# Optimization experiments

Measured on AMD Instinct MI355X. Metric: run time of the kernel, lower is better.

The kernel has to match this reference:

```python
import jax, jax.numpy as jnp
import numpy as np


def _mlp(x, ws, bs):
    # Linear->ReLU between layers, final Linear has no activation
    for i, (w, b) in enumerate(zip(ws, bs)):
        x = x @ w + b
        if i < len(ws) - 1:
            x = jax.nn.relu(x)
    return x


def setup_inputs() -> dict:
    key = jax.random.key(0)
    ks = jax.random.split(key, 24)
    n, q, H, W, dim = 2, 131072, 64, 2048, 64
    num = 4
    depth = jax.random.normal(ks[0], (n, 3, H, W), dtype=jnp.float32)
    feat = jax.random.normal(ks[1], (n, dim, H, W), dtype=jnp.float32)
    coord = jax.random.uniform(ks[2], (n, q, 2), dtype=jnp.float32, minval=-1.0, maxval=1.0)

    def lin(k, din, dout):
        kw, kb = jax.random.split(k)
        s = 1.0 / np.sqrt(din)
        w = jax.random.uniform(kw, (din, dout), minval=-s, maxval=s, dtype=jnp.float32)
        b = jax.random.uniform(kb, (dout,), minval=-s, maxval=s, dtype=jnp.float32)
        return w, b

    # pos_embedd: 2*num=8 -> [dim, num//2*dim] = [64,128] -> num*dim=256
    pe_dims = [2 * num, dim, (num // 2) * dim, num * dim]
    # encoder_xy: num*dim=256 -> [num*dim, num//2*dim, dim] = [256,128,64] -> num=4
    enc_dims = [num * dim, num * dim, (num // 2) * dim, dim, num]
    inp = {"depth": depth, "feat": feat, "coord": coord}
    for i in range(3):
        w, b = lin(ks[3 + i], pe_dims[i], pe_dims[i + 1])
        inp[f"pe_w{i}"] = w
        inp[f"pe_b{i}"] = b
    for i in range(4):
        w, b = lin(ks[8 + i], enc_dims[i], enc_dims[i + 1])
        inp[f"enc_w{i}"] = w
        inp[f"enc_b{i}"] = b
    return inp


def reference(depth, feat, coord,
              pe_w0, pe_b0, pe_w1, pe_b1, pe_w2, pe_b2,
              enc_w0, enc_b0, enc_w1, enc_b1, enc_w2, enc_b2, enc_w3, enc_b3):
    n, C, H, W = feat.shape
    q = coord.shape[1]
    eps = 1e-6
    # xy range-view magnitude map [n, H, W]
    xy = jnp.sqrt(depth[:, 1] ** 2 + depth[:, 2] ** 2)

    rx = 1.0 / H  # 2 / H / 2
    ry = 1.0 / W
    # offsets in the same (vx outer, vy inner) order as the torch loop
    offs = jnp.array([[-1.0, -1.0], [-1.0, 1.0], [1.0, -1.0], [1.0, 1.0]], dtype=coord.dtype)
    shift = offs * jnp.array([rx, ry], dtype=coord.dtype) + eps  # [4,2]
    c = jnp.clip(coord[None] + shift[:, None, None, :], -1.0 + 1e-6, 1.0 - 1e-6)  # [4,n,q,2]

    # nearest grid_sample, align_corners=False: unnormalized = ((g+1)*size - 1)/2, then round
    iy = jnp.clip(jnp.round(((c[..., 0] + 1.0) * H - 1.0) * 0.5).astype(jnp.int32), 0, H - 1)
    ix = jnp.clip(jnp.round(((c[..., 1] + 1.0) * W - 1.0) * 0.5).astype(jnp.int32), 0, W - 1)

    b = jnp.arange(n)[None, :, None]  # broadcasts against [4,n,q]
    q_feat = feat[b, :, iy, ix]      # [4,n,q,C] nearest-gathered features
    pred_xy = xy[b, iy, ix]          # [4,n,q]

    # sampled pixel-center coords (what grid_sample of feat_coord returns)
    qc_y = -1.0 + (2.0 * iy.astype(coord.dtype) + 1.0) / H
    qc_x = -1.0 + (2.0 * ix.astype(coord.dtype) + 1.0) / W
    rel = jnp.stack([(coord[None, ..., 0] - qc_y) * H,
                     (coord[None, ..., 1] - qc_x) * W], axis=-1)  # [4,n,q,2]

    # rearrange 't n q d -> (n q) (t d)'
    qf = q_feat.transpose(1, 2, 0, 3).reshape(n * q, 4 * C)
    rc = rel.transpose(1, 2, 0, 3).reshape(n * q, 4 * 2)

    qf = qf + _mlp(rc, [pe_w0, pe_w1, pe_w2], [pe_b0, pe_b1, pe_b2])
    logits = _mlp(qf, [enc_w0, enc_w1, enc_w2, enc_w3], [enc_b0, enc_b1, enc_b2, enc_b3])  # [nq,4]
    w = jax.nn.softmax(logits, axis=1)

    p = pred_xy.transpose(1, 2, 0).reshape(n * q, 4)  # 't n q -> (n q) t'
    ret = jnp.sum(p * w, axis=1).reshape(n, q, 1)     # [nq,1,4] @ [nq,4,1]
    return ret
```

## Files before the change

kernel.cpp:

```cpp
#include <hip/hip_runtime.h>
#include <hip/hip_runtime_api.h>
#include <math.h>

#define NBATCH 2
#define QQ     131072
#define HH     64
#define WWID   2048
#define CC     64
#define HWSZ   (HH*WWID)

constexpr int ROWS    = 128;
constexpr int THREADS = 256;

constexpr int ASTR_B = 512;

constexpr int OFF_A   = 0;
constexpr int OFF_TAP = 65536;
constexpr int OFF_PXY = OFF_TAP + 2048;
constexpr int OFF_E3  = OFF_PXY + 2048;
constexpr int LDS_BYTES = OFF_E3 + 1024;

constexpr int WOFF_PE0 = 0;
constexpr int WOFF_PE1 = 1024;
constexpr int WOFF_PE2 = 9216;
constexpr int WOFF_E0  = 41984;
constexpr int WOFF_E1  = 107520;
constexpr int WOFF_E2  = 140288;
constexpr int WTOTAL   = 148480;

typedef __attribute__((ext_vector_type(8)))  short bf16x8;
typedef __attribute__((ext_vector_type(16))) float f32x16;

__device__ __forceinline__ ushort f2bf(float f) {
    union { float f; unsigned u; } x; x.f = f;
    unsigned r = x.u + 0x7fffu + ((x.u >> 16) & 1u);
    return (ushort)(r >> 16);
}
__device__ __forceinline__ float bf2f(ushort h) {
    union { unsigned u; float f; } x; x.u = ((unsigned)h) << 16;
    return x.f;
}
__device__ __forceinline__ unsigned cvtpk(float a, float b) {
    unsigned r;
    asm("v_cvt_pk_bf16_f32 %0, %1, %2" : "=v"(r) : "v"(a), "v"(b));
    return r;
}

__device__ __forceinline__ int swA(int row, int colByte) {
    return row * ASTR_B + (colByte ^ ((row & 15) << 4));
}

struct WDesc { const float* src; int K; int N; int kshift; };
struct WPack { WDesc d[6]; };

__global__ __launch_bounds__(256) void prep_weights(WPack p, ushort* __restrict__ dst)
{
    int e = blockIdx.x * 256 + threadIdx.x;
    int off = 0;
    #pragma unroll
    for (int L = 0; L < 6; ++L) {
        const int Kp = 1 << p.d[L].kshift;
        const int N  = p.d[L].N;
        const int sz = N * Kp;
        if (e < sz) {
            const int n = e / Kp;
            const int k = e & (Kp - 1);
            const float v = (k < p.d[L].K) ? p.d[L].src[(size_t)k * N + n] : 0.f;
            const int kstep = k >> 4;
            const int tile  = kstep * (N >> 5) + (n >> 5);
            const int lane  = (n & 31) | (((k >> 3) & 1) << 5);
            const int j     = k & 7;
            dst[off + tile * 512 + lane * 8 + j] = f2bf(v);
            return;
        }
        e -= sz; off += sz;
    }
}

__global__ __launch_bounds__(256) void prep_feat(
    const float* __restrict__ depth, const float* __restrict__ feat,
    ushort* __restrict__ nhwc, float* __restrict__ xy)
{
    const int idx = blockIdx.x * 256 + threadIdx.x;
    const int b   = idx >> 17;
    const int yx  = idx & (HWSZ - 1);

    const float d1 = depth[(b * 3 + 1) * HWSZ + yx];
    const float d2 = depth[(b * 3 + 2) * HWSZ + yx];
    xy[idx] = sqrtf(d1 * d1 + d2 * d2);

    const float* fp = feat + (size_t)b * CC * HWSZ + yx;
    ushort* op = nhwc + (size_t)idx * CC;
    #pragma unroll
    for (int c = 0; c < CC; c += 8) {
        union { uint4 v; ushort u[8]; } t;
        #pragma unroll
        for (int j = 0; j < 8; ++j) t.u[j] = f2bf(fp[(size_t)(c + j) * HWSZ]);
        *(uint4*)(op + c) = t.v;
    }
}

template <int K, int N, bool RELU>
__device__ __forceinline__ void dense_layer(
    char* __restrict__ sA, const ushort* __restrict__ Wt,
    const float* __restrict__ Bg, int tid)
{
    constexpr int CT = (N == 256) ? 2 : 1;
    constexpr int RG = (N == 64) ? 2 : 4;
    constexpr int KS = K / 16;

    const int lane = tid & 63, wv = tid >> 6;
    const int row0 = (N == 64) ? (wv >> 1) * 64 : 0;
    const int col0 = (N == 64) ? (wv & 1) * 32 : wv * (N / 4);
    const int lrow = lane & 31;
    const int lkb  = (lane >> 5) * 16;

    f32x16 acc[RG][CT];
    #pragma unroll
    for (int rg = 0; rg < RG; ++rg)
        #pragma unroll
        for (int ct = 0; ct < CT; ++ct)
            #pragma unroll
            for (int t = 0; t < 16; ++t) acc[rg][ct][t] = 0.f;

    const char* wbase = (const char*)Wt + (size_t)lane * 16;

    for (int kst = 0; kst < KS; ++kst) {
        const int cb = kst * 32 + lkb;
        bf16x8 a[RG];
        #pragma unroll
        for (int rg = 0; rg < RG; ++rg)
            a[rg] = *(const bf16x8*)(sA + swA(row0 + rg * 32 + lrow, cb));
        #pragma unroll
        for (int ct = 0; ct < CT; ++ct) {
            const int tile = kst * (N >> 5) + (col0 >> 5) + ct;
            const bf16x8 bw = *(const bf16x8*)(wbase + tile * 1024);
            #pragma unroll
            for (int rg = 0; rg < RG; ++rg)
                acc[rg][ct] = __builtin_amdgcn_mfma_f32_32x32x16_bf16(bw, a[rg], acc[rg][ct], 0, 0, 0);
        }
    }
    __syncthreads();

    #pragma unroll
    for (int ct = 0; ct < CT; ++ct) {
        #pragma unroll
        for (int q = 0; q < 4; ++q) {
            const int colb = col0 + ct * 32 + q * 8 + (lane >> 5) * 4;
            const float4 b4 = *(const float4*)(Bg + colb);
            #pragma unroll
            for (int rg = 0; rg < RG; ++rg) {
                float v0 = acc[rg][ct][q * 4 + 0] + b4.x;
                float v1 = acc[rg][ct][q * 4 + 1] + b4.y;
                float v2 = acc[rg][ct][q * 4 + 2] + b4.z;
                float v3 = acc[rg][ct][q * 4 + 3] + b4.w;
                if (RELU) {
                    v0 = fmaxf(v0, 0.f); v1 = fmaxf(v1, 0.f);
                    v2 = fmaxf(v2, 0.f); v3 = fmaxf(v3, 0.f);
                }
                uint2 pk;
                pk.x = cvtpk(v0, v1);
                pk.y = cvtpk(v2, v3);
                const int row = row0 + rg * 32 + lrow;
                *(uint2*)(sA + swA(row, colb * 2)) = pk;
            }
        }
    }
    __syncthreads();
}

template <bool USE_WS>
__global__ __launch_bounds__(256, 2) void fused_kernel(
    const float* __restrict__ depth, const float* __restrict__ feat,
    const float* __restrict__ coord,
    const float* __restrict__ pb0, const float* __restrict__ pb1,
    const float* __restrict__ pb2,
    const float* __restrict__ eb0, const float* __restrict__ eb1,
    const float* __restrict__ eb2,
    const float* __restrict__ ew3, const float* __restrict__ eb3,
    const ushort* __restrict__ wt,
    const ushort* __restrict__ nhwc, const float* __restrict__ xyws,
    float* __restrict__ out)
{
    extern __shared__ char lds[];
    char*  sA   = lds + OFF_A;
    int*   sTap = (int*)(lds + OFF_TAP);
    float* sPxy = (float*)(lds + OFF_PXY);
    float* sE3  = (float*)(lds + OFF_E3);

    const int tid  = threadIdx.x;
    const int row0g = blockIdx.x * ROWS;
    const int b     = row0g >> 17;

    sE3[tid] = ew3[tid];

    #pragma unroll
    for (int it = 0; it < 2; ++it) {
        #pragma clang fp contract(off)
        const int item = it * 256 + tid;
        const int r = item >> 2, s = item & 3;
        const int row = row0g + r;
        const float cy = coord[row * 2 + 0];
        const float cx = coord[row * 2 + 1];
        const float offy = (s < 2) ? -1.f : 1.f;
        const float offx = (s & 1) ? 1.f : -1.f;
        const float rx = 1.f / (float)HH, ry = 1.f / (float)WWID;
        float ccy = cy + (offy * rx + 1e-6f);
        float ccx = cx + (offx * ry + 1e-6f);
        ccy = fminf(fmaxf(ccy, -1.f + 1e-6f), 1.f - 1e-6f);
        ccx = fminf(fmaxf(ccx, -1.f + 1e-6f), 1.f - 1e-6f);
        int iy = (int)rintf(((ccy + 1.f) * (float)HH - 1.f) * 0.5f);
        int ix = (int)rintf(((ccx + 1.f) * (float)WWID - 1.f) * 0.5f);
        iy = min(max(iy, 0), HH - 1);
        ix = min(max(ix, 0), WWID - 1);
        const float qcy = -1.f + (2.f * (float)iy + 1.f) / (float)HH;
        const float qcx = -1.f + (2.f * (float)ix + 1.f) / (float)WWID;
        *(ushort*)(sA + swA(r, s * 4 + 0)) = f2bf((cy - qcy) * (float)HH);
        *(ushort*)(sA + swA(r, s * 4 + 2)) = f2bf((cx - qcx) * (float)WWID);
        if (s == 0) {
            uint4 z; z.x = z.y = z.z = z.w = 0u;
            *(uint4*)(sA + swA(r, 16)) = z;
        }
        const int tap = iy * WWID + ix;
        sTap[r * 4 + s] = tap;
        float px;
        if (USE_WS) {
            px = xyws[b * HWSZ + tap];
        } else {
            const float d1 = depth[(b * 3 + 1) * HWSZ + tap];
            const float d2 = depth[(b * 3 + 2) * HWSZ + tap];
            px = sqrtf(d1 * d1 + d2 * d2);
        }
        sPxy[r * 4 + s] = px;
    }
    __syncthreads();

    dense_layer<16,  64,  true >(sA, wt + WOFF_PE0, pb0, tid);
    dense_layer<64,  128, true >(sA, wt + WOFF_PE1, pb1, tid);
    dense_layer<128, 256, false>(sA, wt + WOFF_PE2, pb2, tid);

    #pragma unroll
    for (int it = 0; it < 2; ++it) {
        const int item = it * 256 + tid;
        const int gr = item >> 2, gs = item & 3;
        const int tap = sTap[gr * 4 + gs];
        const int cb0 = gs * 128;
        if (USE_WS) {
            const ushort* src = nhwc + ((size_t)b * HWSZ + tap) * CC;
            #pragma unroll
            for (int g = 0; g < 8; ++g) {
                char* dp = sA + swA(gr, cb0 + g * 16);
                union { uint4 v; ushort u[8]; } a, d;
                a.v = *(const uint4*)(src + g * 8);
                d.v = *(uint4*)dp;
                float s0 = bf2f(a.u[0]) + bf2f(d.u[0]);
                float s1 = bf2f(a.u[1]) + bf2f(d.u[1]);
                float s2 = bf2f(a.u[2]) + bf2f(d.u[2]);
                float s3 = bf2f(a.u[3]) + bf2f(d.u[3]);
                float s4 = bf2f(a.u[4]) + bf2f(d.u[4]);
                float s5 = bf2f(a.u[5]) + bf2f(d.u[5]);
                float s6 = bf2f(a.u[6]) + bf2f(d.u[6]);
                float s7 = bf2f(a.u[7]) + bf2f(d.u[7]);
                uint4 o;
                o.x = cvtpk(s0, s1); o.y = cvtpk(s2, s3);
                o.z = cvtpk(s4, s5); o.w = cvtpk(s6, s7);
                *(uint4*)dp = o;
            }
        } else {
            const float* fp = feat + (size_t)b * CC * HWSZ + tap;
            #pragma unroll 8
            for (int c = 0; c < CC; ++c) {
                ushort* p = (ushort*)(sA + swA(gr, cb0 + c * 2));
                *p = f2bf(bf2f(*p) + fp[(size_t)c * HWSZ]);
            }
        }
    }
    __syncthreads();

    dense_layer<256, 256, true>(sA, wt + WOFF_E0, eb0, tid);
    dense_layer<256, 128, true>(sA, wt + WOFF_E1, eb1, tid);
    dense_layer<128, 64,  true>(sA, wt + WOFF_E2, eb2, tid);

    {
        const int fr = tid >> 1, sub = tid & 1;
        float l0 = 0.f, l1 = 0.f, l2 = 0.f, l3 = 0.f;
        #pragma unroll
        for (int g = 0; g < 4; ++g) {
            union { uint4 v; ushort u[8]; } h;
            h.v = *(const uint4*)(sA + swA(fr, sub * 64 + g * 16));
            #pragma unroll
            for (int kk = 0; kk < 8; ++kk) {
                const float a = bf2f(h.u[kk]);
                const float4 w = ((const float4*)sE3)[sub * 32 + g * 8 + kk];
                l0 = fmaf(a, w.x, l0);
                l1 = fmaf(a, w.y, l1);
                l2 = fmaf(a, w.z, l2);
                l3 = fmaf(a, w.w, l3);
            }
        }
        l0 += __shfl_xor(l0, 1);
        l1 += __shfl_xor(l1, 1);
        l2 += __shfl_xor(l2, 1);
        l3 += __shfl_xor(l3, 1);
        if (sub == 0) {
            l0 += eb3[0]; l1 += eb3[1]; l2 += eb3[2]; l3 += eb3[3];
            const float m  = fmaxf(fmaxf(l0, l1), fmaxf(l2, l3));
            const float e0 = expf(l0 - m), e1 = expf(l1 - m);
            const float e2 = expf(l2 - m), e3 = expf(l3 - m);
            const float inv = 1.f / (e0 + e1 + e2 + e3);
            const float o = (sPxy[fr * 4 + 0] * e0 + sPxy[fr * 4 + 1] * e1 +
                             sPxy[fr * 4 + 2] * e2 + sPxy[fr * 4 + 3] * e3) * inv;
            out[row0g + fr] = o;
        }
    }
}

extern "C" void kernel_launch(void* const* d_in, const int* in_sizes, int n_in,
                              void* d_out, int out_size, void* d_ws, size_t ws_size,
                              hipStream_t stream)
{
    const float* depth = (const float*)d_in[0];
    const float* feat  = (const float*)d_in[1];
    const float* coord = (const float*)d_in[2];
    const float* pw0 = (const float*)d_in[3],  *pb0 = (const float*)d_in[4];
    const float* pw1 = (const float*)d_in[5],  *pb1 = (const float*)d_in[6];
    const float* pw2 = (const float*)d_in[7],  *pb2 = (const float*)d_in[8];
    const float* ew0 = (const float*)d_in[9],  *eb0 = (const float*)d_in[10];
    const float* ew1 = (const float*)d_in[11], *eb1 = (const float*)d_in[12];
    const float* ew2 = (const float*)d_in[13], *eb2 = (const float*)d_in[14];
    const float* ew3 = (const float*)d_in[15], *eb3 = (const float*)d_in[16];
    float* out = (float*)d_out;

    const size_t nhwc_bytes = (size_t)NBATCH * HWSZ * CC * 2;
    const size_t xy_bytes   = (size_t)NBATCH * HWSZ * 4;
    const size_t wt_bytes   = (size_t)WTOTAL * 2;
    const bool use_ws = (ws_size >= nhwc_bytes + xy_bytes + wt_bytes);

    ushort* nhwc = (ushort*)d_ws;
    float*  xyws = (float*)((char*)d_ws + nhwc_bytes);
    ushort* wt   = use_ws ? (ushort*)((char*)d_ws + nhwc_bytes + xy_bytes)
                          : (ushort*)d_ws;

    WPack pack;
    pack.d[0] = { pw0, 8,   64,  4 };
    pack.d[1] = { pw1, 64,  128, 6 };
    pack.d[2] = { pw2, 128, 256, 7 };
    pack.d[3] = { ew0, 256, 256, 8 };
    pack.d[4] = { ew1, 256, 128, 8 };
    pack.d[5] = { ew2, 128, 64,  7 };
    prep_weights<<<WTOTAL / 256, 256, 0, stream>>>(pack, wt);

    const int nblocks = (NBATCH * QQ) / ROWS;

    if (use_ws) {
        prep_feat<<<(NBATCH * HWSZ) / 256, 256, 0, stream>>>(depth, feat, nhwc, xyws);
        hipFuncSetAttribute((const void*)fused_kernel<true>,
                            hipFuncAttributeMaxDynamicSharedMemorySize, LDS_BYTES);
        fused_kernel<true><<<nblocks, THREADS, LDS_BYTES, stream>>>(
            depth, feat, coord, pb0, pb1, pb2, eb0, eb1, eb2, ew3, eb3,
            wt, nhwc, xyws, out);
    } else {
        hipFuncSetAttribute((const void*)fused_kernel<false>,
                            hipFuncAttributeMaxDynamicSharedMemorySize, LDS_BYTES);
        fused_kernel<false><<<nblocks, THREADS, LDS_BYTES, stream>>>(
            depth, feat, coord, pb0, pb1, pb2, eb0, eb1, eb2, ew3, eb3,
            wt, nhwc, xyws, out);
    }
}
```

Measured before the change: 137.4 us.

## Make each wave own 32 rows end-to-end and drop block barriers

Restructures the MLP so each of the four waves processes its own 32 rows through every layer instead of splitting columns across waves. This removes all __syncthreads between layers and the LDS tap table, since taps stay in registers and the final-layer weights are copied once per wave. In exchange each wave reads the full weight matrix for every layer, with no A-fragment reuse across row groups. Per-wave accumulators also grow to N/32 tiles, up to 8 f32x16 for the 256-wide layers, which raises register pressure.

After: 388.3 us. 183% more time.

```diff
diff --git a/kernel.cpp b/kernel.cpp
--- a/kernel.cpp
+++ b/kernel.cpp
@@ -15,10 +15,9 @@
 constexpr int ASTR_B = 512;
 
 constexpr int OFF_A   = 0;
-constexpr int OFF_TAP = 65536;
-constexpr int OFF_PXY = OFF_TAP + 2048;
+constexpr int OFF_PXY = 65536;
 constexpr int OFF_E3  = OFF_PXY + 2048;
-constexpr int LDS_BYTES = OFF_E3 + 1024;
+constexpr int LDS_BYTES = OFF_E3 + 4096;
 
 constexpr int WOFF_PE0 = 0;
 constexpr int WOFF_PE1 = 1024;
@@ -101,72 +100,55 @@
 }
 
 template <int K, int N, bool RELU>
-__device__ __forceinline__ void dense_layer(
+__device__ __forceinline__ void dense_wave(
     char* __restrict__ sA, const ushort* __restrict__ Wt,
-    const float* __restrict__ Bg, int tid)
-{
-    constexpr int CT = (N == 256) ? 2 : 1;
-    constexpr int RG = (N == 64) ? 2 : 4;
+    const float* __restrict__ Bg, int lane, int R0)
+{
+    constexpr int CT = N / 32;
     constexpr int KS = K / 16;
 
-    const int lane = tid & 63, wv = tid >> 6;
-    const int row0 = (N == 64) ? (wv >> 1) * 64 : 0;
-    const int col0 = (N == 64) ? (wv & 1) * 32 : wv * (N / 4);
     const int lrow = lane & 31;
     const int lkb  = (lane >> 5) * 16;
-
-    f32x16 acc[RG][CT];
-    #pragma unroll
-    for (int rg = 0; rg < RG; ++rg)
-        #pragma unroll
-        for (int ct = 0; ct < CT; ++ct)
-            #pragma unroll
-            for (int t = 0; t < 16; ++t) acc[rg][ct][t] = 0.f;
+    const int row  = R0 + lrow;
+
+    f32x16 acc[CT];
+    #pragma unroll
+    for (int ct = 0; ct < CT; ++ct)
+        #pragma unroll
+        for (int t = 0; t < 16; ++t) acc[ct][t] = 0.f;
 
     const char* wbase = (const char*)Wt + (size_t)lane * 16;
 
     for (int kst = 0; kst < KS; ++kst) {
         const int cb = kst * 32 + lkb;
-        bf16x8 a[RG];
-        #pragma unroll
-        for (int rg = 0; rg < RG; ++rg)
-            a[rg] = *(const bf16x8*)(sA + swA(row0 + rg * 32 + lrow, cb));
+        const bf16x8 a = *(const bf16x8*)(sA + swA(row, cb));
         #pragma unroll
         for (int ct = 0; ct < CT; ++ct) {
-            const int tile = kst * (N >> 5) + (col0 >> 5) + ct;
-            const bf16x8 bw = *(const bf16x8*)(wbase + tile * 1024);
-            #pragma unroll
-            for (int rg = 0; rg < RG; ++rg)
-                acc[rg][ct] = __builtin_amdgcn_mfma_f32_32x32x16_bf16(bw, a[rg], acc[rg][ct], 0, 0, 0);
-        }
-    }
-    __syncthreads();
+            const bf16x8 bw = *(const bf16x8*)(wbase + (size_t)(kst * CT + ct) * 1024);
+            acc[ct] = __builtin_amdgcn_mfma_f32_32x32x16_bf16(bw, a, acc[ct], 0, 0, 0);
+        }
+    }
 
     #pragma unroll
     for (int ct = 0; ct < CT; ++ct) {
         #pragma unroll
         for (int q = 0; q < 4; ++q) {
-            const int colb = col0 + ct * 32 + q * 8 + (lane >> 5) * 4;
+            const int colb = ct * 32 + q * 8 + (lane >> 5) * 4;
             const float4 b4 = *(const float4*)(Bg + colb);
-            #pragma unroll
-            for (int rg = 0; rg < RG; ++rg) {
-                float v0 = acc[rg][ct][q * 4 + 0] + b4.x;
-                float v1 = acc[rg][ct][q * 4 + 1] + b4.y;
-                float v2 = acc[rg][ct][q * 4 + 2] + b4.z;
-                float v3 = acc[rg][ct][q * 4 + 3] + b4.w;
-                if (RELU) {
-                    v0 = fmaxf(v0, 0.f); v1 = fmaxf(v1, 0.f);
-                    v2 = fmaxf(v2, 0.f); v3 = fmaxf(v3, 0.f);
-                }
-                uint2 pk;
-                pk.x = cvtpk(v0, v1);
-                pk.y = cvtpk(v2, v3);
-                const int row = row0 + rg * 32 + lrow;
-                *(uint2*)(sA + swA(row, colb * 2)) = pk;
+            float v0 = acc[ct][q * 4 + 0] + b4.x;
+            float v1 = acc[ct][q * 4 + 1] + b4.y;
+            float v2 = acc[ct][q * 4 + 2] + b4.z;
+            float v3 = acc[ct][q * 4 + 3] + b4.w;
+            if (RELU) {
+                v0 = fmaxf(v0, 0.f); v1 = fmaxf(v1, 0.f);
+                v2 = fmaxf(v2, 0.f); v3 = fmaxf(v3, 0.f);
             }
-        }
-    }
-    __syncthreads();
+            uint2 pk;
+            pk.x = cvtpk(v0, v1);
+            pk.y = cvtpk(v2, v3);
+            *(uint2*)(sA + swA(row, colb * 2)) = pk;
+        }
+    }
 }
 
 template <bool USE_WS>
@@ -184,21 +166,23 @@
 {
     extern __shared__ char lds[];
     char*  sA   = lds + OFF_A;
-    int*   sTap = (int*)(lds + OFF_TAP);
     float* sPxy = (float*)(lds + OFF_PXY);
-    float* sE3  = (float*)(lds + OFF_E3);
 
     const int tid  = threadIdx.x;
+    const int lane = tid & 63, wv = tid >> 6;
+    const int R0   = wv * 32;
     const int row0g = blockIdx.x * ROWS;
     const int b     = row0g >> 17;
 
-    sE3[tid] = ew3[tid];
-
+    float4* sE3w = (float4*)(lds + OFF_E3 + wv * 1024);
+    sE3w[lane] = ((const float4*)ew3)[lane];
+
+    int taps[2];
     #pragma unroll
     for (int it = 0; it < 2; ++it) {
         #pragma clang fp contract(off)
-        const int item = it * 256 + tid;
-        const int r = item >> 2, s = item & 3;
+        const int item = it * 64 + lane;
+        const int r = R0 + (item >> 2), s = item & 3;
         const int row = row0g + r;
         const float cy = coord[row * 2 + 0];
         const float cx = coord[row * 2 + 1];
@@ -222,7 +206,7 @@
             *(uint4*)(sA + swA(r, 16)) = z;
         }
         const int tap = iy * WWID + ix;
-        sTap[r * 4 + s] = tap;
+        taps[it] = tap;
         float px;
         if (USE_WS) {
             px = xyws[b * HWSZ + tap];
@@ -233,17 +217,16 @@
         }
         sPxy[r * 4 + s] = px;
     }
-    __syncthreads();
-
-    dense_layer<16,  64,  true >(sA, wt + WOFF_PE0, pb0, tid);
-    dense_layer<64,  128, true >(sA, wt + WOFF_PE1, pb1, tid);
-    dense_layer<128, 256, false>(sA, wt + WOFF_PE2, pb2, tid);
+
+    dense_wave<16,  64,  true >(sA, wt + WOFF_PE0, pb0, lane, R0);
+    dense_wave<64,  128, true >(sA, wt + WOFF_PE1, pb1, lane, R0);
+    dense_wave<128, 256, false>(sA, wt + WOFF_PE2, pb2, lane, R0);
 
     #pragma unroll
     for (int it = 0; it < 2; ++it) {
-        const int item = it * 256 + tid;
-        const int gr = item >> 2, gs = item & 3;
-        const int tap = sTap[gr * 4 + gs];
+        const int item = it * 64 + lane;
+        const int gr = R0 + (item >> 2), gs = item & 3;
+        const int tap = taps[it];
         const int cb0 = gs * 128;
         if (USE_WS) {
             const ushort* src = nhwc + ((size_t)b * HWSZ + tap) * CC;
@@ -275,14 +258,13 @@
             }
         }
     }
-    __syncthreads();
-
-    dense_layer<256, 256, true>(sA, wt + WOFF_E0, eb0, tid);
-    dense_layer<256, 128, true>(sA, wt + WOFF_E1, eb1, tid);
-    dense_layer<128, 64,  true>(sA, wt + WOFF_E2, eb2, tid);
+
+    dense_wave<256, 256, true>(sA, wt + WOFF_E0, eb0, lane, R0);
+    dense_wave<256, 128, true>(sA, wt + WOFF_E1, eb1, lane, R0);
+    dense_wave<128, 64,  true>(sA, wt + WOFF_E2, eb2, lane, R0);
 
     {
-        const int fr = tid >> 1, sub = tid & 1;
+        const int fr = R0 + (lane >> 1), sub = lane & 1;
         float l0 = 0.f, l1 = 0.f, l2 = 0.f, l3 = 0.f;
         #pragma unroll
         for (int g = 0; g < 4; ++g) {
@@ -291,7 +273,7 @@
             #pragma unroll
             for (int kk = 0; kk < 8; ++kk) {
                 const float a = bf2f(h.u[kk]);
-                const float4 w = ((const float4*)sE3)[sub * 32 + g * 8 + kk];
+                const float4 w = sE3w[sub * 32 + g * 8 + kk];
                 l0 = fmaf(a, w.x, l0);
                 l1 = fmaf(a, w.y, l1);
                 l2 = fmaf(a, w.z, l2);
```
